# Performance work log

Measured on AMD Instinct MI355X. Metric: run time of the kernel, lower is better.

Reference implementation:

```python
import jax, jax.numpy as jnp
import numpy as np

EMBED_DIM = 512
U_EMBED = 6
NUM_HEADS = 8
HEAD_DIM = EMBED_DIM // NUM_HEADS
SCALE = HEAD_DIM ** -0.5
BS, N = 8, 1024


def setup_inputs() -> dict:
    key = jax.random.key(0)
    ks = jax.random.split(key, 9)
    x = jax.random.normal(ks[0], (BS, N, EMBED_DIM), dtype=jnp.float32)
    u = jax.random.normal(ks[1], (BS, U_EMBED, N, N), dtype=jnp.float32)
    umask = jax.random.randint(ks[2], (BS, N, N, 1), 0, 2).astype(bool)
    s = EMBED_DIM ** -0.5
    Wq = jax.random.normal(ks[3], (EMBED_DIM, EMBED_DIM), dtype=jnp.float32) * s
    Wk = jax.random.normal(ks[4], (EMBED_DIM, EMBED_DIM), dtype=jnp.float32) * s
    Wv = jax.random.normal(ks[5], (EMBED_DIM, EMBED_DIM), dtype=jnp.float32) * s
    Wu = jax.random.normal(ks[6], (NUM_HEADS, U_EMBED), dtype=jnp.float32) * (U_EMBED ** -0.5)
    bu = jnp.zeros((NUM_HEADS,), dtype=jnp.float32)
    Wo = jax.random.normal(ks[7], (EMBED_DIM, EMBED_DIM), dtype=jnp.float32) * s
    bo = jnp.zeros((EMBED_DIM,), dtype=jnp.float32)
    return {"x": x, "u": u, "umask": umask, "Wq": Wq, "Wk": Wk, "Wv": Wv,
            "Wu": Wu, "bu": bu, "Wo": Wo, "bo": bo}


def reference(x, u, umask, Wq, Wk, Wv, Wu, bu, Wo, bo):
    bs, n, _ = x.shape
    # projections (torch Linear: y = x @ W.T)
    Q = (x @ Wq.T).reshape(bs, n, NUM_HEADS, HEAD_DIM)
    K = (x @ Wk.T).reshape(bs, n, NUM_HEADS, HEAD_DIM)
    V = (x @ Wv.T).reshape(bs, n, NUM_HEADS, HEAD_DIM)
    # scores: [bs, H, N, N]
    scores = jnp.einsum('bqhd,bkhd->bhqk', Q, K) * SCALE
    # 1x1 conv bias: [bs, u_embed, N, N] -> [bs, H, N, N]
    ub = jnp.einsum('bunm,hu->bhnm', u, Wu) + bu[None, :, None, None]
    # umask: [bs, N, N, 1] -> transpose(3,1) -> [bs, 1, N, N]
    m = jnp.transpose(umask, (0, 3, 2, 1))
    ub = jnp.where(m, -jnp.inf, ub)
    scores = scores + ub
    attn = jax.nn.softmax(scores, axis=-1)
    ctx = jnp.einsum('bhqk,bkhd->bqhd', attn, V).reshape(bs, n, EMBED_DIM)
    out = ctx @ Wo.T + bo
    return out, attn
```

## Files before the change

kernel.cpp:

```cpp
#include <hip/hip_runtime.h>
#include <hip/hip_bf16.h>
#include <math.h>

#define BSZ 8
#define SEQ 1024
#define EMB 512
#define NH 8
#define HD 64
#define UE 6
#define QKSCALE 0.125f

typedef unsigned short u16;
typedef short bf16x8 __attribute__((ext_vector_type(8)));
typedef float f32x4 __attribute__((ext_vector_type(4)));
typedef unsigned short ushort4_t __attribute__((ext_vector_type(4)));

__device__ __forceinline__ u16 f2bf(float f) {
  unsigned u = __float_as_uint(f);
  unsigned r = (u + 0x7fffu + ((u >> 16) & 1u)) >> 16;
  return (u16)r;
}
__device__ __forceinline__ float bf2f(u16 v) {
  return __uint_as_float(((unsigned)v) << 16);
}
__device__ __forceinline__ void f2hl(float f, u16& hi, u16& lo) {
  hi = f2bf(f);
  float fh = __uint_as_float(((unsigned)hi) << 16);
  lo = f2bf(f - fh);
}
#define F2HL_V(fv, hv, lv, idx)            \
  {                                        \
    u16 _h, _l;                            \
    f2hl((fv), _h, _l);                    \
    (hv)[idx] = (short)_h;                 \
    (lv)[idx] = (short)_l;                 \
  }
__device__ __forceinline__ f32x4 mfma_bf16(bf16x8 a, bf16x8 b, f32x4 c) {
  return __builtin_amdgcn_mfma_f32_16x16x32_bf16(a, b, c, 0, 0, 0);
}

__global__ __launch_bounds__(256) void split_kernel(const float* __restrict__ src,
                                                    u16* __restrict__ hi, u16* __restrict__ lo, int n4) {
  int i = blockIdx.x * 256 + threadIdx.x;
  if (i >= n4) return;
  float4 v = ((const float4*)src)[i];
  ushort4_t h, l;
  F2HL_V(v.x, h, l, 0); F2HL_V(v.y, h, l, 1);
  F2HL_V(v.z, h, l, 2); F2HL_V(v.w, h, l, 3);
  ((ushort4_t*)hi)[i] = h;
  ((ushort4_t*)lo)[i] = l;
}

__global__ __launch_bounds__(256, 2) void qkv_mfma_kernel(
    const u16* __restrict__ Xhi, const u16* __restrict__ Xlo, const u16* __restrict__ Wsp,
    u16* __restrict__ Qhi, u16* __restrict__ Qlo,
    u16* __restrict__ Khi, u16* __restrict__ Klo, u16* __restrict__ Vt) {
  const int mt = blockIdx.x, h = blockIdx.y, wsel = blockIdx.z;
  const int m0 = mt * 64, c0 = h * 64;
  const u16* __restrict__ WH = Wsp + (size_t)wsel * 524288;
  const u16* __restrict__ WL = WH + 262144;
  __shared__ u16 AH[64][40], AL[64][40], BH[64][40], BL[64][40];
  __shared__ u16 vout[64][69];
  const int t = threadIdx.x, w = t >> 6, l = t & 63;
  const int wr = (w >> 1) * 32, wc = (w & 1) * 32;
  f32x4 acc[2][2] = {};
  const int srow = t >> 2;
  for (int e0 = 0; e0 < EMB; e0 += 32) {
    {
      const int c = (t & 3) * 8;
      *(bf16x8*)&AH[srow][c] = *(const bf16x8*)&Xhi[(size_t)(m0 + srow) * EMB + e0 + c];
      *(bf16x8*)&AL[srow][c] = *(const bf16x8*)&Xlo[(size_t)(m0 + srow) * EMB + e0 + c];
      *(bf16x8*)&BH[srow][c] = *(const bf16x8*)&WH[(size_t)(c0 + srow) * EMB + e0 + c];
      *(bf16x8*)&BL[srow][c] = *(const bf16x8*)&WL[(size_t)(c0 + srow) * EMB + e0 + c];
    }
    __syncthreads();
    const int ar = l & 15, ach = (l >> 4) << 3;
    bf16x8 ah0 = *(bf16x8*)&AH[wr + ar][ach],      ah1 = *(bf16x8*)&AH[wr + 16 + ar][ach];
    bf16x8 al0 = *(bf16x8*)&AL[wr + ar][ach],      al1 = *(bf16x8*)&AL[wr + 16 + ar][ach];
    bf16x8 bh0 = *(bf16x8*)&BH[wc + ar][ach],      bh1 = *(bf16x8*)&BH[wc + 16 + ar][ach];
    bf16x8 bl0 = *(bf16x8*)&BL[wc + ar][ach],      bl1 = *(bf16x8*)&BL[wc + 16 + ar][ach];
    acc[0][0] = mfma_bf16(ah0, bh0, acc[0][0]); acc[0][0] = mfma_bf16(ah0, bl0, acc[0][0]); acc[0][0] = mfma_bf16(al0, bh0, acc[0][0]);
    acc[0][1] = mfma_bf16(ah0, bh1, acc[0][1]); acc[0][1] = mfma_bf16(ah0, bl1, acc[0][1]); acc[0][1] = mfma_bf16(al0, bh1, acc[0][1]);
    acc[1][0] = mfma_bf16(ah1, bh0, acc[1][0]); acc[1][0] = mfma_bf16(ah1, bl0, acc[1][0]); acc[1][0] = mfma_bf16(al1, bh0, acc[1][0]);
    acc[1][1] = mfma_bf16(ah1, bh1, acc[1][1]); acc[1][1] = mfma_bf16(ah1, bl1, acc[1][1]); acc[1][1] = mfma_bf16(al1, bh1, acc[1][1]);
    __syncthreads();
  }
  const int bb = m0 >> 10, n0 = m0 & 1023;
  if (wsel < 2) {
    u16* __restrict__ OH = wsel ? Khi : Qhi;
    u16* __restrict__ OL = wsel ? Klo : Qlo;
#pragma unroll
    for (int i = 0; i < 2; ++i)
#pragma unroll
      for (int j = 0; j < 2; ++j) {
        const int col = wc + 16 * j + (l & 15);
#pragma unroll
        for (int r = 0; r < 4; ++r) {
          const int n = n0 + wr + 16 * i + ((l >> 4) << 2) + r;
          size_t o = ((size_t)(bb * NH + h) * SEQ + n) * HD + col;
          u16 hi, lo; f2hl(acc[i][j][r], hi, lo);
          OH[o] = hi; OL[o] = lo;
        }
      }
  } else {
#pragma unroll
    for (int i = 0; i < 2; ++i)
#pragma unroll
      for (int j = 0; j < 2; ++j) {
        const int col = wc + 16 * j + (l & 15);
#pragma unroll
        for (int r = 0; r < 4; ++r)
          vout[wr + 16 * i + ((l >> 4) << 2) + r][col] = f2bf(acc[i][j][r]);
      }
    __syncthreads();
    const int d = t >> 2, nch = (t & 3) * 16;
    bf16x8 o0, o1;
#pragma unroll
    for (int i = 0; i < 8; ++i) o0[i] = (short)vout[nch + i][d];
#pragma unroll
    for (int i = 0; i < 8; ++i) o1[i] = (short)vout[nch + 8 + i][d];
    size_t dst = ((size_t)(bb * NH + h) * HD + d) * SEQ + n0 + nch;
    *(bf16x8*)&Vt[dst] = o0;
    *(bf16x8*)&Vt[dst + 8] = o1;
  }
}

__global__ __launch_bounds__(256, 2) void scores_kernel(
    const u16* __restrict__ Qhi, const u16* __restrict__ Qlo,
    const u16* __restrict__ Khi, const u16* __restrict__ Klo,
    const float* __restrict__ u, const int* __restrict__ umask,
    const float* __restrict__ Wu, const float* __restrict__ bu,
    u16* __restrict__ praw, float* __restrict__ sums) {
  const int kt = blockIdx.x, qt = blockIdx.y, b = blockIdx.z;
  const int q0 = qt * 64, k0 = kt * 64;
  __shared__ u16 KsH[2][64][68], KsL[2][64][68];
  __shared__ unsigned char ms[64][68];
  const int t = threadIdx.x, w = t >> 6, l = t & 63;
  const int kl = l & 15, g = l >> 4;
  const int qb = 16 * w + (g << 2);

#pragma unroll
  for (int r = 0; r < 16; ++r) {
    int idx = r * 256 + t; int k = idx >> 6, q = idx & 63;
    ms[k][q] = (unsigned char)(umask[((size_t)b * SEQ + k0 + k) * SEQ + q0 + q] != 0);
  }

  unsigned upk[UE][4][2];
  const float* ubase = u + ((size_t)b * UE * SEQ + q0 + qb) * SEQ + k0 + kl;
#pragma unroll
  for (int uu = 0; uu < UE; ++uu)
#pragma unroll
    for (int tt = 0; tt < 4; ++tt)
#pragma unroll
      for (int p = 0; p < 2; ++p) {
        const float* up = ubase + (size_t)uu * SEQ * SEQ + (size_t)(2 * p) * SEQ + 16 * tt;
        upk[uu][tt][p] = (unsigned)f2bf(up[0]) | ((unsigned)f2bf(up[SEQ]) << 16);
      }

  const int krow_s = t >> 2, kc_s = (t & 3) * 16;
  bf16x8 preH[2][2], preL[2][2];
#pragma unroll
  for (int h2 = 0; h2 < 2; ++h2) {
    const u16* kp = Khi + ((size_t)(b * NH + h2) * SEQ + k0 + krow_s) * HD + kc_s;
    const u16* kq = Klo + ((size_t)(b * NH + h2) * SEQ + k0 + krow_s) * HD + kc_s;
    preH[h2][0] = *(const bf16x8*)kp; preH[h2][1] = *(const bf16x8*)(kp + 8);
    preL[h2][0] = *(const bf16x8*)kq; preL[h2][1] = *(const bf16x8*)(kq + 8);
  }

  for (int hp = 0; hp < 4; ++hp) {
    const int h0 = hp * 2;
    __syncthreads();
#pragma unroll
    for (int h2 = 0; h2 < 2; ++h2) {
      *(bf16x8*)&KsH[h2][krow_s][kc_s] = preH[h2][0];
      *(bf16x8*)&KsH[h2][krow_s][kc_s + 8] = preH[h2][1];
      *(bf16x8*)&KsL[h2][krow_s][kc_s] = preL[h2][0];
      *(bf16x8*)&KsL[h2][krow_s][kc_s + 8] = preL[h2][1];
    }
    if (hp < 3) {
#pragma unroll
      for (int h2 = 0; h2 < 2; ++h2) {
        const u16* kp = Khi + ((size_t)(b * NH + h0 + 2 + h2) * SEQ + k0 + krow_s) * HD + kc_s;
        const u16* kq = Klo + ((size_t)(b * NH + h0 + 2 + h2) * SEQ + k0 + krow_s) * HD + kc_s;
        preH[h2][0] = *(const bf16x8*)kp; preH[h2][1] = *(const bf16x8*)(kp + 8);
        preL[h2][0] = *(const bf16x8*)kq; preL[h2][1] = *(const bf16x8*)(kq + 8);
      }
    }
    __syncthreads();

    bf16x8 qh[2][2], qo[2][2];
    float wu_[2][UE], bub[2];
    u16* pbase[2];
#pragma unroll
    for (int h2 = 0; h2 < 2; ++h2) {
      const int bh = b * NH + h0 + h2;
      const u16* qp = Qhi + ((size_t)bh * SEQ + q0 + 16 * w + kl) * HD + (g << 3);
      const u16* qq = Qlo + ((size_t)bh * SEQ + q0 + 16 * w + kl) * HD + (g << 3);
      qh[h2][0] = *(const bf16x8*)qp; qh[h2][1] = *(const bf16x8*)(qp + 32);
      qo[h2][0] = *(const bf16x8*)qq; qo[h2][1] = *(const bf16x8*)(qq + 32);
#pragma unroll
      for (int uu = 0; uu < UE; ++uu) wu_[h2][uu] = Wu[(h0 + h2) * UE + uu];
      bub[h2] = bu[h0 + h2];
      pbase[h2] = praw + ((size_t)(bh * SEQ + q0 + qb)) * 2048 + 1024 + k0 + kl;
    }

    float esum[2][4] = {};
#pragma unroll
    for (int tt = 0; tt < 4; ++tt) {
      const int krow = tt * 16 + kl, kch = g << 3;
      bf16x8 kh00 = *(bf16x8*)&KsH[0][krow][kch], kh01 = *(bf16x8*)&KsH[0][krow][kch + 32];
      bf16x8 kb00 = *(bf16x8*)&KsL[0][krow][kch], kb01 = *(bf16x8*)&KsL[0][krow][kch + 32];
      bf16x8 kh10 = *(bf16x8*)&KsH[1][krow][kch], kh11 = *(bf16x8*)&KsH[1][krow][kch + 32];
      bf16x8 kb10 = *(bf16x8*)&KsL[1][krow][kch], kb11 = *(bf16x8*)&KsL[1][krow][kch + 32];
      f32x4 a0 = {0.f, 0.f, 0.f, 0.f}, a1 = {0.f, 0.f, 0.f, 0.f};
      a0 = mfma_bf16(qh[0][0], kh00, a0);  a1 = mfma_bf16(qh[1][0], kh10, a1);
      a0 = mfma_bf16(qh[0][1], kh01, a0);  a1 = mfma_bf16(qh[1][1], kh11, a1);
      a0 = mfma_bf16(qh[0][0], kb00, a0);  a1 = mfma_bf16(qh[1][0], kb10, a1);
      a0 = mfma_bf16(qh[0][1], kb01, a0);  a1 = mfma_bf16(qh[1][1], kb11, a1);
      a0 = mfma_bf16(qo[0][0], kh00, a0);  a1 = mfma_bf16(qo[1][0], kh10, a1);
      a0 = mfma_bf16(qo[0][1], kh01, a0);  a1 = mfma_bf16(qo[1][1], kh11, a1);
#pragma unroll
      for (int p = 0; p < 2; ++p) {
        float ub0x = bub[0], ub0y = bub[0], ub1x = bub[1], ub1y = bub[1];
#pragma unroll
        for (int uu = 0; uu < UE; ++uu) {
          unsigned pk = upk[uu][tt][p];
          float flo = __uint_as_float(pk << 16);
          float fhi = __uint_as_float(pk & 0xffff0000u);
          ub0x = fmaf(wu_[0][uu], flo, ub0x); ub0y = fmaf(wu_[0][uu], fhi, ub0y);
          ub1x = fmaf(wu_[1][uu], flo, ub1x); ub1y = fmaf(wu_[1][uu], fhi, ub1y);
        }
        const unsigned char m0 = ms[tt * 16 + kl][qb + 2 * p];
        const unsigned char m1 = ms[tt * 16 + kl][qb + 2 * p + 1];
        u16 e00 = m0 ? (u16)0 : f2bf(__expf(a0[2 * p] * QKSCALE + ub0x));
        u16 e01 = m1 ? (u16)0 : f2bf(__expf(a0[2 * p + 1] * QKSCALE + ub0y));
        u16 e10 = m0 ? (u16)0 : f2bf(__expf(a1[2 * p] * QKSCALE + ub1x));
        u16 e11 = m1 ? (u16)0 : f2bf(__expf(a1[2 * p + 1] * QKSCALE + ub1y));
        pbase[0][(size_t)(2 * p) * 2048 + tt * 16]     = e00;
        pbase[0][(size_t)(2 * p + 1) * 2048 + tt * 16] = e01;
        pbase[1][(size_t)(2 * p) * 2048 + tt * 16]     = e10;
        pbase[1][(size_t)(2 * p + 1) * 2048 + tt * 16] = e11;
        esum[0][2 * p]     += bf2f(e00);
        esum[0][2 * p + 1] += bf2f(e01);
        esum[1][2 * p]     += bf2f(e10);
        esum[1][2 * p + 1] += bf2f(e11);
      }
    }
#pragma unroll
    for (int h2 = 0; h2 < 2; ++h2)
#pragma unroll
      for (int r = 0; r < 4; ++r) {
#pragma unroll
        for (int o = 1; o <= 8; o <<= 1) esum[h2][r] += __shfl_xor(esum[h2][r], o);
      }
    if (kl == 0) {
#pragma unroll
      for (int h2 = 0; h2 < 2; ++h2)
#pragma unroll
        for (int r = 0; r < 4; ++r)
          sums[((size_t)(b * NH + h0 + h2) * SEQ + q0 + qb + r) * 16 + kt] = esum[h2][r];
    }
  }
}

__global__ __launch_bounds__(256, 4) void pv_softmax_kernel(
    float* attn, const u16* __restrict__ Vt,
    const float* __restrict__ sums, u16* __restrict__ ctx) {
  const int qt = blockIdx.x, bh = blockIdx.y;
  const int q0 = qt * 64;
  __shared__ u16 Pl[64][72], Vs[64][72];
  __shared__ float invl[64];
  const int t = threadIdx.x, w = t >> 6, l = t & 63;
  const int row = t >> 2, cc = (t & 3) * 16;

  float S = 0.f;
  {
    const float* sp = sums + ((size_t)bh * SEQ + q0 + row) * 16 + (t & 3) * 4;
#pragma unroll
    for (int j = 0; j < 4; ++j) S += sp[j];
#pragma unroll
    for (int o = 1; o <= 2; o <<= 1) S += __shfl_xor(S, o);
  }
  const float inv = 1.0f / S;
  if ((t & 3) == 0) invl[row] = inv;

  const u16* prow = (const u16*)attn + ((size_t)(bh * SEQ + q0 + row)) * 2048 + 1024;
  float* arow = attn + ((size_t)(bh * SEQ + q0 + row)) * SEQ;
  const u16* vrow = Vt + ((size_t)bh * HD + row) * SEQ + cc;

  const int wr = (w >> 1) * 32, wc = (w & 1) * 32;
  f32x4 acc[2][2] = {};
  bf16x8 pa = *(const bf16x8*)&prow[cc], pb = *(const bf16x8*)&prow[cc + 8];
  bf16x8 vb0 = *(const bf16x8*)vrow, vb1 = *(const bf16x8*)(vrow + 8);

  for (int k0 = 0; k0 < SEQ; k0 += 64) {
    float* ap = arow + k0 + cc;
    {
      float4 o0, o1, o2, o3;
      o0.x = bf2f((u16)pa[0]) * inv; o0.y = bf2f((u16)pa[1]) * inv;
      o0.z = bf2f((u16)pa[2]) * inv; o0.w = bf2f((u16)pa[3]) * inv;
      o1.x = bf2f((u16)pa[4]) * inv; o1.y = bf2f((u16)pa[5]) * inv;
      o1.z = bf2f((u16)pa[6]) * inv; o1.w = bf2f((u16)pa[7]) * inv;
      o2.x = bf2f((u16)pb[0]) * inv; o2.y = bf2f((u16)pb[1]) * inv;
      o2.z = bf2f((u16)pb[2]) * inv; o2.w = bf2f((u16)pb[3]) * inv;
      o3.x = bf2f((u16)pb[4]) * inv; o3.y = bf2f((u16)pb[5]) * inv;
      o3.z = bf2f((u16)pb[6]) * inv; o3.w = bf2f((u16)pb[7]) * inv;
      ((float4*)ap)[0] = o0; ((float4*)ap)[1] = o1;
      ((float4*)ap)[2] = o2; ((float4*)ap)[3] = o3;
    }
    *(bf16x8*)&Pl[row][cc] = pa;
    *(bf16x8*)&Pl[row][cc + 8] = pb;
    *(bf16x8*)&Vs[row][cc] = vb0;
    *(bf16x8*)&Vs[row][cc + 8] = vb1;

    if (k0 + 64 < SEQ) {
      pa = *(const bf16x8*)&prow[k0 + 64 + cc];
      pb = *(const bf16x8*)&prow[k0 + 64 + cc + 8];
      vb0 = *(const bf16x8*)(vrow + k0 + 64);
      vb1 = *(const bf16x8*)(vrow + k0 + 72);
    }
    __syncthreads();
#pragma unroll
    for (int kb = 0; kb < 2; ++kb) {
      const int kch = kb * 32 + ((l >> 4) << 3);
      bf16x8 a0 = *(bf16x8*)&Pl[wr + (l & 15)][kch];
      bf16x8 a1 = *(bf16x8*)&Pl[wr + 16 + (l & 15)][kch];
      bf16x8 b0 = *(bf16x8*)&Vs[wc + (l & 15)][kch];
      bf16x8 b1 = *(bf16x8*)&Vs[wc + 16 + (l & 15)][kch];
      acc[0][0] = mfma_bf16(a0, b0, acc[0][0]);
      acc[0][1] = mfma_bf16(a0, b1, acc[0][1]);
      acc[1][0] = mfma_bf16(a1, b0, acc[1][0]);
      acc[1][1] = mfma_bf16(a1, b1, acc[1][1]);
    }
    __syncthreads();
  }
  const int b = bh >> 3, h = bh & 7;
#pragma unroll
  for (int i = 0; i < 2; ++i)
#pragma unroll
    for (int j = 0; j < 2; ++j) {
      const int d = h * HD + wc + 16 * j + (l & 15);
#pragma unroll
      for (int r = 0; r < 4; ++r) {
        const int ql_ = wr + 16 * i + ((l >> 4) << 2) + r;
        ctx[((size_t)(b * SEQ + q0 + ql_)) * EMB + d] = f2bf(acc[i][j][r] * invl[ql_]);
      }
    }
}

__global__ __launch_bounds__(256, 2) void oproj_kernel(
    const u16* __restrict__ ctx,
    const u16* __restrict__ WoH, const u16* __restrict__ WoL,
    const float* __restrict__ bo, float* __restrict__ out) {
  const int mt = blockIdx.x, ct = blockIdx.y;
  const int m0 = mt * 64, c0 = ct * 64;
  __shared__ u16 AH[64][40], BH[64][40], BL[64][40];
  const int t = threadIdx.x, w = t >> 6, l = t & 63;
  const int wr = (w >> 1) * 32, wc = (w & 1) * 32;
  f32x4 acc[2][2] = {};
  const int srow = t >> 2, sc = (t & 3) * 8;
  for (int e0 = 0; e0 < EMB; e0 += 32) {
    *(bf16x8*)&AH[srow][sc] = *(const bf16x8*)&ctx[(size_t)(m0 + srow) * EMB + e0 + sc];
    *(bf16x8*)&BH[srow][sc] = *(const bf16x8*)&WoH[(size_t)(c0 + srow) * EMB + e0 + sc];
    *(bf16x8*)&BL[srow][sc] = *(const bf16x8*)&WoL[(size_t)(c0 + srow) * EMB + e0 + sc];
    __syncthreads();
    const int ar = l & 15, ach = (l >> 4) << 3;
    bf16x8 ah0 = *(bf16x8*)&AH[wr + ar][ach],      ah1 = *(bf16x8*)&AH[wr + 16 + ar][ach];
    bf16x8 bh0 = *(bf16x8*)&BH[wc + ar][ach],      bh1 = *(bf16x8*)&BH[wc + 16 + ar][ach];
    bf16x8 bl0 = *(bf16x8*)&BL[wc + ar][ach],      bl1 = *(bf16x8*)&BL[wc + 16 + ar][ach];
    acc[0][0] = mfma_bf16(ah0, bh0, acc[0][0]); acc[0][0] = mfma_bf16(ah0, bl0, acc[0][0]);
    acc[0][1] = mfma_bf16(ah0, bh1, acc[0][1]); acc[0][1] = mfma_bf16(ah0, bl1, acc[0][1]);
    acc[1][0] = mfma_bf16(ah1, bh0, acc[1][0]); acc[1][0] = mfma_bf16(ah1, bl0, acc[1][0]);
    acc[1][1] = mfma_bf16(ah1, bh1, acc[1][1]); acc[1][1] = mfma_bf16(ah1, bl1, acc[1][1]);
    __syncthreads();
  }
#pragma unroll
  for (int i = 0; i < 2; ++i)
#pragma unroll
    for (int j = 0; j < 2; ++j) {
      const int col = c0 + wc + 16 * j + (l & 15);
      const float bias = bo[col];
#pragma unroll
      for (int r = 0; r < 4; ++r) {
        const int m = m0 + wr + 16 * i + ((l >> 4) << 2) + r;
        out[(size_t)m * EMB + col] = acc[i][j][r] + bias;
      }
    }
}

extern "C" void kernel_launch(void* const* d_in, const int* in_sizes, int n_in,
                              void* d_out, int out_size, void* d_ws, size_t ws_size,
                              hipStream_t stream) {
  const float* x = (const float*)d_in[0];
  const float* u = (const float*)d_in[1];
  const int* umask = (const int*)d_in[2];
  const float* Wq = (const float*)d_in[3];
  const float* Wk = (const float*)d_in[4];
  const float* Wv = (const float*)d_in[5];
  const float* Wu = (const float*)d_in[6];
  const float* bu = (const float*)d_in[7];
  const float* Wo = (const float*)d_in[8];
  const float* bo = (const float*)d_in[9];

  float* out = (float*)d_out;
  float* attn = out + (size_t)BSZ * SEQ * EMB;

  const size_t per = (size_t)BSZ * NH * SEQ * HD;
  u16* ws = (u16*)d_ws;
  u16* Qhi = ws;
  u16* Qlo = Qhi + per;
  u16* Khi = Qlo + per;
  u16* Klo = Khi + per;
  u16* Vt = Klo + per;
  u16* ctx = Vt + per;
  float* sums = (float*)(ctx + per);
  u16* Wsp = (u16*)(sums + (size_t)BSZ * NH * SEQ * 16);

  u16* Xhi = (u16*)attn;
  u16* Xlo = Xhi + (size_t)BSZ * SEQ * EMB;

  const int wn4 = 262144 / 4;
  split_kernel<<<dim3(wn4 / 256), 256, 0, stream>>>(Wq, Wsp + 0 * 524288, Wsp + 0 * 524288 + 262144, wn4);
  split_kernel<<<dim3(wn4 / 256), 256, 0, stream>>>(Wk, Wsp + 1 * 524288, Wsp + 1 * 524288 + 262144, wn4);
  split_kernel<<<dim3(wn4 / 256), 256, 0, stream>>>(Wv, Wsp + 2 * 524288, Wsp + 2 * 524288 + 262144, wn4);
  split_kernel<<<dim3(wn4 / 256), 256, 0, stream>>>(Wo, Wsp + 3 * 524288, Wsp + 3 * 524288 + 262144, wn4);
  const int xn4 = (int)((size_t)BSZ * SEQ * EMB / 4);
  split_kernel<<<dim3(xn4 / 256), 256, 0, stream>>>(x, Xhi, Xlo, xn4);

  qkv_mfma_kernel<<<dim3(128, 8, 3), 256, 0, stream>>>(Xhi, Xlo, Wsp, Qhi, Qlo, Khi, Klo, Vt);
  scores_kernel<<<dim3(16, 16, 8), 256, 0, stream>>>(Qhi, Qlo, Khi, Klo, u, umask, Wu, bu,
                                                     (u16*)attn, sums);
  pv_softmax_kernel<<<dim3(16, 64), 256, 0, stream>>>(attn, Vt, sums, ctx);
  oproj_kernel<<<dim3(128, 8), 256, 0, stream>>>(ctx, Wsp + 3 * 524288, Wsp + 3 * 524288 + 262144, bo, out);
}
```

Measured before the change: 430.4 us.

## Stage score outputs through LDS for vectorized stores and reload u per tile

Exponentiated scores are now written into a per-wave shared-memory tile and then stored to global memory as 16-byte vector writes per row, replacing scattered 2-byte stores. The u bias values are no longer preloaded and packed to bf16 in registers up front. They are instead loaded as fp32 inside each key subtile iteration and for every head pair. This cuts register pressure and drops the bf16 rounding of u, but it re-reads u from global memory four times (once per head pair). The LDS staging adds shared-memory traffic, and it relies on the wave's own accesses for ordering since no barrier is placed between the writes and the reads.

```diff
diff --git a/kernel.cpp b/kernel.cpp
--- a/kernel.cpp
+++ b/kernel.cpp
@@ -135,6 +135,7 @@
   const int q0 = qt * 64, k0 = kt * 64;
   __shared__ u16 KsH[2][64][68], KsL[2][64][68];
   __shared__ unsigned char ms[64][68];
+  __shared__ u16 TrB[4][2][16][72];
   const int t = threadIdx.x, w = t >> 6, l = t & 63;
   const int kl = l & 15, g = l >> 4;
   const int qb = 16 * w + (g << 2);
@@ -145,17 +146,7 @@
     ms[k][q] = (unsigned char)(umask[((size_t)b * SEQ + k0 + k) * SEQ + q0 + q] != 0);
   }
 
-  unsigned upk[UE][4][2];
   const float* ubase = u + ((size_t)b * UE * SEQ + q0 + qb) * SEQ + k0 + kl;
-#pragma unroll
-  for (int uu = 0; uu < UE; ++uu)
-#pragma unroll
-    for (int tt = 0; tt < 4; ++tt)
-#pragma unroll
-      for (int p = 0; p < 2; ++p) {
-        const float* up = ubase + (size_t)uu * SEQ * SEQ + (size_t)(2 * p) * SEQ + 16 * tt;
-        upk[uu][tt][p] = (unsigned)f2bf(up[0]) | ((unsigned)f2bf(up[SEQ]) << 16);
-      }
 
   const int krow_s = t >> 2, kc_s = (t & 3) * 16;
   bf16x8 preH[2][2], preL[2][2];
@@ -167,6 +158,8 @@
     preL[h2][0] = *(const bf16x8*)kq; preL[h2][1] = *(const bf16x8*)(kq + 8);
   }
 
+  const int rr = l >> 2, cg = (l & 3) * 16;
+
   for (int hp = 0; hp < 4; ++hp) {
     const int h0 = hp * 2;
     __syncthreads();
@@ -190,7 +183,6 @@
 
     bf16x8 qh[2][2], qo[2][2];
     float wu_[2][UE], bub[2];
-    u16* pbase[2];
 #pragma unroll
     for (int h2 = 0; h2 < 2; ++h2) {
       const int bh = b * NH + h0 + h2;
@@ -201,12 +193,20 @@
 #pragma unroll
       for (int uu = 0; uu < UE; ++uu) wu_[h2][uu] = Wu[(h0 + h2) * UE + uu];
       bub[h2] = bu[h0 + h2];
-      pbase[h2] = praw + ((size_t)(bh * SEQ + q0 + qb)) * 2048 + 1024 + k0 + kl;
     }
 
     float esum[2][4] = {};
 #pragma unroll
     for (int tt = 0; tt < 4; ++tt) {
+      float uf[UE][2][2];
+#pragma unroll
+      for (int uu = 0; uu < UE; ++uu)
+#pragma unroll
+        for (int p = 0; p < 2; ++p) {
+          const float* up = ubase + (size_t)uu * SEQ * SEQ + (size_t)(2 * p) * SEQ + 16 * tt;
+          uf[uu][p][0] = up[0];
+          uf[uu][p][1] = up[SEQ];
+        }
       const int krow = tt * 16 + kl, kch = g << 3;
       bf16x8 kh00 = *(bf16x8*)&KsH[0][krow][kch], kh01 = *(bf16x8*)&KsH[0][krow][kch + 32];
       bf16x8 kb00 = *(bf16x8*)&KsL[0][krow][kch], kb01 = *(bf16x8*)&KsL[0][krow][kch + 32];
@@ -224,9 +224,8 @@
         float ub0x = bub[0], ub0y = bub[0], ub1x = bub[1], ub1y = bub[1];
 #pragma unroll
         for (int uu = 0; uu < UE; ++uu) {
-          unsigned pk = upk[uu][tt][p];
-          float flo = __uint_as_float(pk << 16);
-          float fhi = __uint_as_float(pk & 0xffff0000u);
+          const float flo = uf[uu][p][0];
+          const float fhi = uf[uu][p][1];
           ub0x = fmaf(wu_[0][uu], flo, ub0x); ub0y = fmaf(wu_[0][uu], fhi, ub0y);
           ub1x = fmaf(wu_[1][uu], flo, ub1x); ub1y = fmaf(wu_[1][uu], fhi, ub1y);
         }
@@ -236,15 +235,23 @@
         u16 e01 = m1 ? (u16)0 : f2bf(__expf(a0[2 * p + 1] * QKSCALE + ub0y));
         u16 e10 = m0 ? (u16)0 : f2bf(__expf(a1[2 * p] * QKSCALE + ub1x));
         u16 e11 = m1 ? (u16)0 : f2bf(__expf(a1[2 * p + 1] * QKSCALE + ub1y));
-        pbase[0][(size_t)(2 * p) * 2048 + tt * 16]     = e00;
-        pbase[0][(size_t)(2 * p + 1) * 2048 + tt * 16] = e01;
-        pbase[1][(size_t)(2 * p) * 2048 + tt * 16]     = e10;
-        pbase[1][(size_t)(2 * p + 1) * 2048 + tt * 16] = e11;
+        TrB[w][0][(g << 2) + 2 * p][tt * 16 + kl]     = e00;
+        TrB[w][0][(g << 2) + 2 * p + 1][tt * 16 + kl] = e01;
+        TrB[w][1][(g << 2) + 2 * p][tt * 16 + kl]     = e10;
+        TrB[w][1][(g << 2) + 2 * p + 1][tt * 16 + kl] = e11;
         esum[0][2 * p]     += bf2f(e00);
         esum[0][2 * p + 1] += bf2f(e01);
         esum[1][2 * p]     += bf2f(e10);
         esum[1][2 * p + 1] += bf2f(e11);
       }
+    }
+#pragma unroll
+    for (int h2 = 0; h2 < 2; ++h2) {
+      bf16x8 v0 = *(bf16x8*)&TrB[w][h2][rr][cg];
+      bf16x8 v1 = *(bf16x8*)&TrB[w][h2][rr][cg + 8];
+      u16* pp = praw + ((size_t)((b * NH + h0 + h2) * SEQ + q0 + 16 * w + rr)) * 2048 + 1024 + k0 + cg;
+      *(bf16x8*)pp = v0;
+      *(bf16x8*)(pp + 8) = v1;
     }
 #pragma unroll
     for (int h2 = 0; h2 < 2; ++h2)
```

After: 376.4 us (median of 2 runs). 1.14x faster.
